# Kernel optimization log

Measured on AMD Instinct MI355X. Metric: run time of the kernel, lower is better.

The kernel has to match this reference:

```python
import jax, jax.numpy as jnp
import numpy as np

N_NODES = 32_000
N_EDGES = 512_000
D_NODE_IN = 3
D_EDGE_IN = 3
LATENT = 32
HIDDEN = 128
MP_ITERS = 4
D_OUT = 1


def _w(key, shape):
    # fan-in scaled init (lecun-normal-ish), fan_in is the second-to-last dim
    return jax.random.normal(key, shape, jnp.float32) / jnp.sqrt(jnp.float32(shape[-2]))


def _mlp(x, w0, w1, w2):
    # MLP with nb_layers=2 hidden relu layers + linear output, no biases
    return jax.nn.relu(jax.nn.relu(x @ w0) @ w1) @ w2


def setup_inputs() -> dict:
    key = jax.random.key(0)
    ks = jax.random.split(key, 32)
    inp = {
        "input_node": jax.random.normal(ks[0], (N_NODES, D_NODE_IN), jnp.float32),
        "input_edge": jax.random.normal(ks[1], (N_EDGES, D_EDGE_IN), jnp.float32),
        "graph_index": jax.random.randint(ks[2], (N_EDGES, 2), 0, N_NODES, jnp.int32),
        # node encoder: D_NODE_IN -> H -> H -> LATENT
        "enc_n_w0": _w(ks[3], (D_NODE_IN, HIDDEN)),
        "enc_n_w1": _w(ks[4], (HIDDEN, HIDDEN)),
        "enc_n_w2": _w(ks[5], (HIDDEN, LATENT)),
        # edge encoder: D_EDGE_IN -> H -> H -> LATENT
        "enc_e_w0": _w(ks[6], (D_EDGE_IN, HIDDEN)),
        "enc_e_w1": _w(ks[7], (HIDDEN, HIDDEN)),
        "enc_e_w2": _w(ks[8], (HIDDEN, LATENT)),
        # per-iteration edge processor MLP: 3*LATENT -> H -> H -> LATENT (stacked over MP_ITERS)
        "ep_w0": _w(ks[9], (MP_ITERS, 3 * LATENT, HIDDEN)),
        "ep_w1": _w(ks[10], (MP_ITERS, HIDDEN, HIDDEN)),
        "ep_w2": _w(ks[11], (MP_ITERS, HIDDEN, LATENT)),
        # per-iteration node processor MLP: 2*LATENT -> H -> H -> LATENT
        "np_w0": _w(ks[12], (MP_ITERS, 2 * LATENT, HIDDEN)),
        "np_w1": _w(ks[13], (MP_ITERS, HIDDEN, HIDDEN)),
        "np_w2": _w(ks[14], (MP_ITERS, HIDDEN, LATENT)),
        # node decoder: LATENT -> H -> H -> D_OUT
        "dec_w0": _w(ks[15], (LATENT, HIDDEN)),
        "dec_w1": _w(ks[16], (HIDDEN, HIDDEN)),
        "dec_w2": _w(ks[17], (HIDDEN, D_OUT)),
    }
    return inp


def reference(input_node, input_edge, graph_index,
              enc_n_w0, enc_n_w1, enc_n_w2,
              enc_e_w0, enc_e_w1, enc_e_w2,
              ep_w0, ep_w1, ep_w2,
              np_w0, np_w1, np_w2,
              dec_w0, dec_w1, dec_w2):
    senders = graph_index[:, 0]
    receivers = graph_index[:, 1]
    n_nodes = input_node.shape[0]

    node = _mlp(input_node, enc_n_w0, enc_n_w1, enc_n_w2)  # [N, LATENT]
    edge = _mlp(input_edge, enc_e_w0, enc_e_w1, enc_e_w2)  # [E, LATENT]

    def step(carry, ws):
        node, edge = carry
        ew0, ew1, ew2, nw0, nw1, nw2 = ws
        # edge update: concat(edge, node[sender], node[receiver]) -> MLP -> residual
        e_in = jnp.concatenate([edge, node[senders], node[receivers]], axis=-1)
        edge = _mlp(e_in, ew0, ew1, ew2) + edge
        # jraph aggregates edges to nodes; NodeProcessor uses only received aggregation
        recv_agg = jax.ops.segment_sum(edge, receivers, num_segments=n_nodes)
        n_in = jnp.concatenate([node, recv_agg], axis=-1)
        node = _mlp(n_in, nw0, nw1, nw2) + node
        return (node, edge), None

    (node, edge), _ = jax.lax.scan(
        step, (node, edge), (ep_w0, ep_w1, ep_w2, np_w0, np_w1, np_w2))

    return _mlp(node, dec_w0, dec_w1, dec_w2)  # [N, D_OUT]
```

## Files before the change

### kernel.cpp

```cpp
#include <hip/hip_runtime.h>

typedef __attribute__((ext_vector_type(8))) _Float16 f16x8;
typedef __attribute__((ext_vector_type(4))) _Float16 f16x4;
typedef __attribute__((ext_vector_type(4))) float f32x4;

#define DI __device__ __forceinline__
#define BAR() asm volatile("s_waitcnt lgkmcnt(0)\n\ts_barrier" ::: "memory")

DI f32x4 mfma16(f16x8 a, f16x8 b, f32x4 c) {
    return __builtin_amdgcn_mfma_f32_16x16x32_f16(a, b, c, 0, 0, 0);
}


template <int NK>
DI void load_wf2(const _Float16* __restrict__ wt, int Kp, int nbase, int l16, int q,
                 f16x8 f[NK][2]) {
#pragma unroll
    for (int nt = 0; nt < 2; ++nt) {
        int n = nbase + nt * 16 + l16;
#pragma unroll
        for (int ks = 0; ks < NK; ++ks)
            f[ks][nt] = *(const f16x8*)(wt + n * Kp + ks * 32 + q * 8);
    }
}

template <int NK0, int MH>
DI void l01(const f16x8 (*w0f)[2], const f16x8 (*w1f)[2],
            const _Float16* __restrict__ X, int xstride,
            _Float16* __restrict__ H0, _Float16* __restrict__ H1,
            int l16, int w, int q) {
    const f32x4 zero = {0.f, 0.f, 0.f, 0.f};
    f32x4 acc[2][MH];
#pragma unroll
    for (int nt = 0; nt < 2; ++nt)
#pragma unroll
        for (int mt = 0; mt < MH; ++mt) acc[nt][mt] = zero;
#pragma unroll
    for (int ks = 0; ks < NK0; ++ks) {
        f16x8 x[MH];
#pragma unroll
        for (int mt = 0; mt < MH; ++mt)
            x[mt] = *(const f16x8*)(X + (mt * 16 + l16) * xstride + ks * 32 + q * 8);
#pragma unroll
        for (int nt = 0; nt < 2; ++nt)
#pragma unroll
            for (int mt = 0; mt < MH; ++mt)
                acc[nt][mt] = mfma16(w0f[ks][nt], x[mt], acc[nt][mt]);
    }
#pragma unroll
    for (int mt = 0; mt < MH; ++mt)
#pragma unroll
        for (int nt = 0; nt < 2; ++nt) {
            f16x4 h;
#pragma unroll
            for (int i = 0; i < 4; ++i) h[i] = (_Float16)fmaxf(acc[nt][mt][i], 0.f);
            *(f16x4*)(H0 + (mt * 16 + l16) * 136 + w * 32 + nt * 16 + q * 4) = h;
        }
    BAR();
    f32x4 a1[2][MH];
#pragma unroll
    for (int nt = 0; nt < 2; ++nt)
#pragma unroll
        for (int mt = 0; mt < MH; ++mt) a1[nt][mt] = zero;
#pragma unroll
    for (int ks = 0; ks < 4; ++ks) {
        f16x8 x[MH];
#pragma unroll
        for (int mt = 0; mt < MH; ++mt)
            x[mt] = *(const f16x8*)(H0 + (mt * 16 + l16) * 136 + ks * 32 + q * 8);
#pragma unroll
        for (int nt = 0; nt < 2; ++nt)
#pragma unroll
            for (int mt = 0; mt < MH; ++mt)
                a1[nt][mt] = mfma16(w1f[ks][nt], x[mt], a1[nt][mt]);
    }
#pragma unroll
    for (int mt = 0; mt < MH; ++mt)
#pragma unroll
        for (int nt = 0; nt < 2; ++nt) {
            f16x4 h;
#pragma unroll
            for (int i = 0; i < 4; ++i) h[i] = (_Float16)fmaxf(a1[nt][mt][i], 0.f);
            *(f16x4*)(H1 + (mt * 16 + l16) * 136 + w * 32 + nt * 16 + q * 4) = h;
        }
    BAR();
}

DI f32x4 l2g(const f16x8* w2f, const _Float16* __restrict__ H1, int l16, int w,
             int q, int g) {
    int m = (w >> 1) * 16 + l16 + 32 * g;
    f32x4 acc = {0.f, 0.f, 0.f, 0.f};
#pragma unroll
    for (int ks = 0; ks < 4; ++ks) {
        f16x8 x = *(const f16x8*)(H1 + m * 136 + ks * 32 + q * 8);
        acc = mfma16(w2f[ks], x, acc);
    }
    return acc;
}

struct WPtrs { const float* p[15]; };

__global__ void k_prep(WPtrs wp, _Float16* __restrict__ ws) {
    int b = blockIdx.x;
    const float* src; int K, N, Np, Kp, off;
    if (b == 0)       { src = wp.p[0];  K = 3;   N = 128; Np = 128; Kp = 32;  off = 0; }
    else if (b == 1)  { src = wp.p[1];  K = 128; N = 128; Np = 128; Kp = 128; off = 4096; }
    else if (b == 2)  { src = wp.p[2];  K = 128; N = 32;  Np = 32;  Kp = 128; off = 20480; }
    else if (b == 3)  { src = wp.p[3];  K = 3;   N = 128; Np = 128; Kp = 32;  off = 24576; }
    else if (b == 4)  { src = wp.p[4];  K = 128; N = 128; Np = 128; Kp = 128; off = 28672; }
    else if (b == 5)  { src = wp.p[5];  K = 128; N = 32;  Np = 32;  Kp = 128; off = 45056; }
    else if (b <= 9)  { int t = b - 6;  src = wp.p[6] + t * 12288;  K = 96;  N = 128; Np = 128; Kp = 96;  off = 49152 + t * 32768; }
    else if (b <= 13) { int t = b - 10; src = wp.p[7] + t * 16384;  K = 128; N = 128; Np = 128; Kp = 128; off = 61440 + t * 32768; }
    else if (b <= 17) { int t = b - 14; src = wp.p[8] + t * 4096;   K = 128; N = 32;  Np = 32;  Kp = 128; off = 77824 + t * 32768; }
    else if (b <= 21) { int t = b - 18; src = wp.p[9] + t * 8192;   K = 64;  N = 128; Np = 128; Kp = 64;  off = 180224 + t * 28672; }
    else if (b <= 25) { int t = b - 22; src = wp.p[10] + t * 16384; K = 128; N = 128; Np = 128; Kp = 128; off = 188416 + t * 28672; }
    else if (b <= 29) { int t = b - 26; src = wp.p[11] + t * 4096;  K = 128; N = 32;  Np = 32;  Kp = 128; off = 204800 + t * 28672; }
    else if (b == 30) { src = wp.p[12]; K = 32;  N = 128; Np = 128; Kp = 32;  off = 294912; }
    else if (b == 31) { src = wp.p[13]; K = 128; N = 128; Np = 128; Kp = 128; off = 299008; }
    else              { src = wp.p[14]; K = 128; N = 1;   Np = 16;  Kp = 128; off = 315392; }
    int total = Np * Kp;
    for (int i = threadIdx.x; i < total; i += 256) {
        int n = i / Kp, k = i - n * Kp;
        float v = (k < K && n < N) ? src[k * N + n] : 0.f;
        ws[off + i] = (_Float16)v;
    }
}

__global__ void k_zero(unsigned* __restrict__ p, int n) {
    int i = blockIdx.x * 256 + threadIdx.x;
    if (i < n) p[i] = 0u;
}
__global__ void k_hist(const int* __restrict__ gi, unsigned* __restrict__ cnt) {
    int e = blockIdx.x * 256 + threadIdx.x;
    if (e < 512000) atomicAdd(&cnt[gi[2 * e + 1]], 1u);
}
__global__ __launch_bounds__(1024) void k_scan(
    const unsigned* __restrict__ cnt, unsigned* __restrict__ rowptr,
    unsigned* __restrict__ cursor) {
    __shared__ unsigned s[1024];
    int t = threadIdx.x;
    unsigned loc[32];
    unsigned sum = 0;
#pragma unroll
    for (int i = 0; i < 32; ++i) {
        int idx = t * 32 + i;
        unsigned v = (idx < 32000) ? cnt[idx] : 0u;
        loc[i] = v; sum += v;
    }
    s[t] = sum;
    __syncthreads();
#pragma unroll
    for (int d = 1; d < 1024; d <<= 1) {
        unsigned x = (t >= d) ? s[t - d] : 0u;
        __syncthreads();
        s[t] += x;
        __syncthreads();
    }
    if (t == 1023) rowptr[32000] = s[1023];
    unsigned off = (t == 0) ? 0u : s[t - 1];
#pragma unroll
    for (int i = 0; i < 32; ++i) {
        int idx = t * 32 + i;
        if (idx < 32000) { rowptr[idx] = off; cursor[idx] = off; off += loc[i]; }
    }
}
__global__ void k_scatter(const int* __restrict__ gi, unsigned* __restrict__ cursor,
                          unsigned* __restrict__ iperm, int2* __restrict__ sr) {
    int e = blockIdx.x * 256 + threadIdx.x;
    if (e < 512000) {
        int s = gi[2 * e], r = gi[2 * e + 1];
        unsigned pos = atomicAdd(&cursor[r], 1u);
        iperm[pos] = (unsigned)e;
        sr[pos] = make_int2(s, r);
    }
}

__global__ __launch_bounds__(256, 3) void k_enc(
    const float* __restrict__ in, _Float16* __restrict__ out,
    const _Float16* __restrict__ w0t, const _Float16* __restrict__ w1t,
    const _Float16* __restrict__ w2t, int NT, const unsigned* __restrict__ iperm) {
    __shared__ __align__(16) _Float16 Xp[64 * 40];
    __shared__ __align__(16) _Float16 H0[64 * 136];
    __shared__ __align__(16) _Float16 H1[64 * 136];
    const int tid = threadIdx.x, w = tid >> 6, lane = tid & 63;
    const int q = lane >> 4, l16 = lane & 15;
    f16x8 w0f[1][2], w1f[4][2], w2f[4];
    load_wf2<1>(w0t, 32, w * 32, l16, q, w0f);
    load_wf2<4>(w1t, 128, w * 32, l16, q, w1f);
    {
        int n2 = (w & 1) * 16 + l16;
#pragma unroll
        for (int ks = 0; ks < 4; ++ks)
            w2f[ks] = *(const f16x8*)(w2t + n2 * 128 + ks * 32 + q * 8);
    }
    for (int c = tid; c < 2560; c += 256) Xp[c] = (_Float16)0.f;
    BAR();

    const int g = gridDim.x;
    const int dr = tid / 3, dc = tid - dr * 3;
    const int orow = (w >> 1) * 16 + l16, ocol = (w & 1) * 16 + q * 4;
    int t = blockIdx.x;

    while (true) {
        if (tid < 192) {
            unsigned e = iperm ? iperm[t * 64 + dr] : (unsigned)(t * 64 + dr);
            Xp[dr * 40 + dc] = (_Float16)in[e * 3 + dc];
        }
        BAR();
        l01<1, 4>(w0f, w1f, Xp, 40, H0, H1, l16, w, q);
#pragma unroll
        for (int gg = 0; gg < 2; ++gg) {
            f32x4 o = l2g(w2f, H1, l16, w, q, gg);
            f16x4 ov;
#pragma unroll
            for (int i = 0; i < 4; ++i) ov[i] = (_Float16)o[i];
            *(f16x4*)(out + (t * 64 + gg * 32 + orow) * 32 + ocol) = ov;
        }
        t += g;
        if (t >= NT) break;
    }
}

__global__ __launch_bounds__(256, 3) void k_edge(
    const _Float16* __restrict__ node, _Float16* __restrict__ edgeP,
    const int2* __restrict__ sr,
    const _Float16* __restrict__ w0t, const _Float16* __restrict__ w1t,
    const _Float16* __restrict__ w2t) {
    __shared__ __align__(16) _Float16 Xe[64 * 104];
    __shared__ __align__(16) _Float16 H0[64 * 136];
    __shared__ __align__(16) _Float16 H1[64 * 136];
    const int tid = threadIdx.x, w = tid >> 6, lane = tid & 63;
    const int q = lane >> 4, l16 = lane & 15;
    f16x8 w0f[3][2], w1f[4][2], w2f[4];
    load_wf2<3>(w0t, 96, w * 32, l16, q, w0f);
    load_wf2<4>(w1t, 128, w * 32, l16, q, w1f);
    {
        int n2 = (w & 1) * 16 + l16;
#pragma unroll
        for (int ks = 0; ks < 4; ++ks)
            w2f[ks] = *(const f16x8*)(w2t + n2 * 128 + ks * 32 + q * 8);
    }
    int cr[3], cs[3];
#pragma unroll
    for (int j = 0; j < 3; ++j) {
        int c = tid + 256 * j;
        cr[j] = c / 12; cs[j] = c - cr[j] * 12;
    }
    const int orow = (w >> 1) * 16 + l16, ocol = (w & 1) * 16 + q * 4;

    const int NT = 8000, g = gridDim.x;
    int t = blockIdx.x;
    int2 srv[3];
#pragma unroll
    for (int j = 0; j < 3; ++j) srv[j] = sr[t * 64 + cr[j]];

    while (true) {
        int tn = t + g; if (tn >= NT) tn = t;
        int4 v[3];
#pragma unroll
        for (int j = 0; j < 3; ++j) {
            int s = cs[j];
            const _Float16* src = (s < 4) ? edgeP + (t * 64 + cr[j]) * 32 + s * 8
                               : (s < 8) ? node + srv[j].x * 32 + (s - 4) * 8
                                         : node + srv[j].y * 32 + (s - 8) * 8;
            v[j] = *(const int4*)src;
        }
        int2 srn[3];
#pragma unroll
        for (int j = 0; j < 3; ++j) srn[j] = sr[tn * 64 + cr[j]];
#pragma unroll
        for (int j = 0; j < 3; ++j)
            *(int4*)(Xe + cr[j] * 104 + cs[j] * 8) = v[j];
        BAR();
        f16x4 oldv[2];
#pragma unroll
        for (int gg = 0; gg < 2; ++gg)
            oldv[gg] = *(const f16x4*)(Xe + (gg * 32 + orow) * 104 + ocol);

        l01<3, 4>(w0f, w1f, Xe, 104, H0, H1, l16, w, q);
#pragma unroll
        for (int gg = 0; gg < 2; ++gg) {
            f32x4 o = l2g(w2f, H1, l16, w, q, gg);
            f16x4 nv;
#pragma unroll
            for (int i = 0; i < 4; ++i) nv[i] = (_Float16)(o[i] + (float)oldv[gg][i]);
            *(f16x4*)(edgeP + (t * 64 + gg * 32 + orow) * 32 + ocol) = nv;
        }

        if (tn == t) break;
        t = tn;
#pragma unroll
        for (int j = 0; j < 3; ++j) srv[j] = srn[j];
    }
}

__global__ __launch_bounds__(256, 3) void k_node(
    _Float16* __restrict__ node, const _Float16* __restrict__ edgeP,
    const unsigned* __restrict__ rowptr,
    const _Float16* __restrict__ w0t, const _Float16* __restrict__ w1t,
    const _Float16* __restrict__ w2t) {
    __shared__ __align__(16) _Float16 Xn[32 * 72];
    __shared__ __align__(16) _Float16 H0[32 * 136];
    __shared__ __align__(16) _Float16 H1[32 * 136];
    const int tid = threadIdx.x, w = tid >> 6, lane = tid & 63;
    const int q = lane >> 4, l16 = lane & 15;
    f16x8 w0f[2][2], w1f[4][2], w2f[4];
    load_wf2<2>(w0t, 64, w * 32, l16, q, w0f);
    load_wf2<4>(w1t, 128, w * 32, l16, q, w1f);
    {
        int n2 = (w & 1) * 16 + l16;
#pragma unroll
        for (int ks = 0; ks < 4; ++ks)
            w2f[ks] = *(const f16x8*)(w2t + n2 * 128 + ks * 32 + q * 8);
    }
    const int t = blockIdx.x;
    const int orow = (w >> 1) * 16 + l16, ocol = (w & 1) * 16 + q * 4;
    {
        int cr = tid >> 3, cs = tid & 7;
        int r = t * 32 + cr;
        if (cs < 4) {
            *(int4*)(Xn + cr * 72 + cs * 8) = *(const int4*)(node + r * 32 + cs * 8);
        } else {
            unsigned b = rowptr[r], e = rowptr[r + 1];
            const _Float16* base = edgeP + (cs - 4) * 8;
            float a0[8], a1[8];
#pragma unroll
            for (int i = 0; i < 8; ++i) { a0[i] = 0.f; a1[i] = 0.f; }
            unsigned p = b;
            for (; p + 2 <= e; p += 2) {
                f16x8 x0 = *(const f16x8*)(base + (p + 0) * 32);
                f16x8 x1 = *(const f16x8*)(base + (p + 1) * 32);
#pragma unroll
                for (int i = 0; i < 8; ++i) { a0[i] += (float)x0[i]; a1[i] += (float)x1[i]; }
            }
            if (p < e) {
                f16x8 x0 = *(const f16x8*)(base + p * 32);
#pragma unroll
                for (int i = 0; i < 8; ++i) a0[i] += (float)x0[i];
            }
            f16x8 h;
#pragma unroll
            for (int i = 0; i < 8; ++i) h[i] = (_Float16)(a0[i] + a1[i]);
            *(f16x8*)(Xn + cr * 72 + cs * 8) = h;
        }
    }
    BAR();
    f16x4 oldv = *(const f16x4*)(Xn + orow * 72 + ocol);
    l01<2, 2>(w0f, w1f, Xn, 72, H0, H1, l16, w, q);
    f32x4 o = l2g(w2f, H1, l16, w, q, 0);
    f16x4 nv;
#pragma unroll
    for (int i = 0; i < 4; ++i) nv[i] = (_Float16)(o[i] + (float)oldv[i]);
    *(f16x4*)(node + (t * 32 + orow) * 32 + ocol) = nv;
}

__global__ __launch_bounds__(256, 3) void k_dec(
    const _Float16* __restrict__ node,
    const _Float16* __restrict__ w0t, const _Float16* __restrict__ w1t,
    const _Float16* __restrict__ w2t, float* __restrict__ out) {
    __shared__ __align__(16) _Float16 Xd[64 * 40];
    __shared__ __align__(16) _Float16 H0[64 * 136];
    __shared__ __align__(16) _Float16 H1[64 * 136];
    const int tid = threadIdx.x, w = tid >> 6, lane = tid & 63;
    const int q = lane >> 4, l16 = lane & 15;
    f16x8 w0f[1][2], w1f[4][2], w2f[4];
    load_wf2<1>(w0t, 32, w * 32, l16, q, w0f);
    load_wf2<4>(w1t, 128, w * 32, l16, q, w1f);
    {
        int n2 = l16;
#pragma unroll
        for (int ks = 0; ks < 4; ++ks)
            w2f[ks] = *(const f16x8*)(w2t + n2 * 128 + ks * 32 + q * 8);
    }
    const int t = blockIdx.x;
    {
        int cr = tid >> 2, cs = tid & 3;
        *(int4*)(Xd + cr * 40 + cs * 8) = *(const int4*)(node + (t * 64 + cr) * 32 + cs * 8);
    }
    BAR();
    l01<1, 4>(w0f, w1f, Xd, 40, H0, H1, l16, w, q);
#pragma unroll
    for (int gg = 0; gg < 2; ++gg) {
        f32x4 o = l2g(w2f, H1, l16, w, q, gg);
        if ((w & 1) == 0 && q == 0) out[t * 64 + gg * 32 + (w >> 1) * 16 + l16] = o[0];
    }
}

extern "C" void kernel_launch(void* const* d_in, const int* in_sizes, int n_in,
                              void* d_out, int out_size, void* d_ws, size_t ws_size,
                              hipStream_t stream) {
    const float* input_node = (const float*)d_in[0];
    const float* input_edge = (const float*)d_in[1];
    const int* gi = (const int*)d_in[2];

    _Float16* ws = (_Float16*)d_ws;
    _Float16* node = (_Float16*)((char*)d_ws + 655360);
    _Float16* edgeP = (_Float16*)((char*)d_ws + 2703360);
    unsigned* rowptr = (unsigned*)((char*)d_ws + 35471360);
    unsigned* cursor = (unsigned*)((char*)d_ws + 35599616);
    unsigned* iperm = (unsigned*)((char*)d_ws + 35727616);
    int2* sr = (int2*)((char*)d_ws + 37775616);

    WPtrs wp;
    for (int i = 0; i < 15; ++i) wp.p[i] = (const float*)d_in[3 + i];

    k_prep<<<33, 256, 0, stream>>>(wp, ws);

    k_zero<<<125, 256, 0, stream>>>(cursor, 32000);
    k_hist<<<2000, 256, 0, stream>>>(gi, cursor);
    k_scan<<<1, 1024, 0, stream>>>(cursor, rowptr, cursor);
    k_scatter<<<2000, 256, 0, stream>>>(gi, cursor, iperm, sr);

    k_enc<<<500, 256, 0, stream>>>(input_node, node, ws + 0, ws + 4096, ws + 20480,
                                   500, nullptr);
    k_enc<<<768, 256, 0, stream>>>(input_edge, edgeP, ws + 24576, ws + 28672,
                                   ws + 45056, 8000, iperm);

    for (int t = 0; t < 4; ++t) {
        k_edge<<<768, 256, 0, stream>>>(node, edgeP, sr,
                                        ws + 49152 + t * 32768,
                                        ws + 61440 + t * 32768,
                                        ws + 77824 + t * 32768);
        k_node<<<1000, 256, 0, stream>>>(node, edgeP, rowptr,
                                         ws + 180224 + t * 28672,
                                         ws + 188416 + t * 28672,
                                         ws + 204800 + t * 28672);
    }
    k_dec<<<500, 256, 0, stream>>>(node, ws + 294912, ws + 299008, ws + 315392,
                                   (float*)d_out);
}
```

Before: 503.9 us.

## Alias input staging buffer onto H1 LDS to raise occupancy to 4 blocks/CU

Each MLP kernel now stages its input tile in the H1 shared buffer instead of a separate LDS array, cutting LDS per block so launch bounds can ask for 4 blocks per CU. Grids grow to 1024 for the edge kernels. The node kernel moves to 64-row tiles so it shares the same LDS layout. Because the staging buffer is reused, the persistent loops need an extra barrier per tile, and k_edge drops its prefetch of the next tile's sender/receiver indices. The extra occupancy is meant to hide the latency of the gathers and global loads, at the cost of more register pressure and lost prefetch.

```diff
diff --git a/kernel.cpp b/kernel.cpp
--- a/kernel.cpp
+++ b/kernel.cpp
@@ -175,13 +175,13 @@
     }
 }
 
-__global__ __launch_bounds__(256, 3) void k_enc(
+__global__ __launch_bounds__(256, 4) void k_enc(
     const float* __restrict__ in, _Float16* __restrict__ out,
     const _Float16* __restrict__ w0t, const _Float16* __restrict__ w1t,
     const _Float16* __restrict__ w2t, int NT, const unsigned* __restrict__ iperm) {
-    __shared__ __align__(16) _Float16 Xp[64 * 40];
     __shared__ __align__(16) _Float16 H0[64 * 136];
-    __shared__ __align__(16) _Float16 H1[64 * 136];
+    __shared__ __align__(16) _Float16 H1s[64 * 136];
+    _Float16* const Xp = H1s;
     const int tid = threadIdx.x, w = tid >> 6, lane = tid & 63;
     const int q = lane >> 4, l16 = lane & 15;
     f16x8 w0f[1][2], w1f[4][2], w2f[4];
@@ -193,24 +193,27 @@
         for (int ks = 0; ks < 4; ++ks)
             w2f[ks] = *(const f16x8*)(w2t + n2 * 128 + ks * 32 + q * 8);
     }
-    for (int c = tid; c < 2560; c += 256) Xp[c] = (_Float16)0.f;
-    BAR();
-
     const int g = gridDim.x;
-    const int dr = tid / 3, dc = tid - dr * 3;
+    const int cr = tid >> 2, csx = tid & 3;
     const int orow = (w >> 1) * 16 + l16, ocol = (w & 1) * 16 + q * 4;
     int t = blockIdx.x;
 
     while (true) {
-        if (tid < 192) {
-            unsigned e = iperm ? iperm[t * 64 + dr] : (unsigned)(t * 64 + dr);
-            Xp[dr * 40 + dc] = (_Float16)in[e * 3 + dc];
-        }
+        f16x8 h;
+#pragma unroll
+        for (int i = 0; i < 8; ++i) h[i] = (_Float16)0.f;
+        if (csx == 0) {
+            unsigned e = iperm ? iperm[t * 64 + cr] : (unsigned)(t * 64 + cr);
+            h[0] = (_Float16)in[e * 3 + 0];
+            h[1] = (_Float16)in[e * 3 + 1];
+            h[2] = (_Float16)in[e * 3 + 2];
+        }
+        *(f16x8*)(Xp + cr * 40 + csx * 8) = h;
         BAR();
-        l01<1, 4>(w0f, w1f, Xp, 40, H0, H1, l16, w, q);
+        l01<1, 4>(w0f, w1f, Xp, 40, H0, H1s, l16, w, q);
 #pragma unroll
         for (int gg = 0; gg < 2; ++gg) {
-            f32x4 o = l2g(w2f, H1, l16, w, q, gg);
+            f32x4 o = l2g(w2f, H1s, l16, w, q, gg);
             f16x4 ov;
 #pragma unroll
             for (int i = 0; i < 4; ++i) ov[i] = (_Float16)o[i];
@@ -218,17 +221,18 @@
         }
         t += g;
         if (t >= NT) break;
-    }
-}
-
-__global__ __launch_bounds__(256, 3) void k_edge(
+        BAR();
+    }
+}
+
+__global__ __launch_bounds__(256, 4) void k_edge(
     const _Float16* __restrict__ node, _Float16* __restrict__ edgeP,
     const int2* __restrict__ sr,
     const _Float16* __restrict__ w0t, const _Float16* __restrict__ w1t,
     const _Float16* __restrict__ w2t) {
-    __shared__ __align__(16) _Float16 Xe[64 * 104];
     __shared__ __align__(16) _Float16 H0[64 * 136];
-    __shared__ __align__(16) _Float16 H1[64 * 136];
+    __shared__ __align__(16) _Float16 H1s[64 * 136];
+    _Float16* const Xe = H1s;
     const int tid = threadIdx.x, w = tid >> 6, lane = tid & 63;
     const int q = lane >> 4, l16 = lane & 15;
     f16x8 w0f[3][2], w1f[4][2], w2f[4];
@@ -250,12 +254,11 @@
 
     const int NT = 8000, g = gridDim.x;
     int t = blockIdx.x;
-    int2 srv[3];
-#pragma unroll
-    for (int j = 0; j < 3; ++j) srv[j] = sr[t * 64 + cr[j]];
 
     while (true) {
-        int tn = t + g; if (tn >= NT) tn = t;
+        int2 srv[3];
+#pragma unroll
+        for (int j = 0; j < 3; ++j) srv[j] = sr[t * 64 + cr[j]];
         int4 v[3];
 #pragma unroll
         for (int j = 0; j < 3; ++j) {
@@ -265,9 +268,6 @@
                                          : node + srv[j].y * 32 + (s - 8) * 8;
             v[j] = *(const int4*)src;
         }
-        int2 srn[3];
-#pragma unroll
-        for (int j = 0; j < 3; ++j) srn[j] = sr[tn * 64 + cr[j]];
 #pragma unroll
         for (int j = 0; j < 3; ++j)
             *(int4*)(Xe + cr[j] * 104 + cs[j] * 8) = v[j];
@@ -277,31 +277,30 @@
         for (int gg = 0; gg < 2; ++gg)
             oldv[gg] = *(const f16x4*)(Xe + (gg * 32 + orow) * 104 + ocol);
 
-        l01<3, 4>(w0f, w1f, Xe, 104, H0, H1, l16, w, q);
+        l01<3, 4>(w0f, w1f, Xe, 104, H0, H1s, l16, w, q);
 #pragma unroll
         for (int gg = 0; gg < 2; ++gg) {
-            f32x4 o = l2g(w2f, H1, l16, w, q, gg);
+            f32x4 o = l2g(w2f, H1s, l16, w, q, gg);
             f16x4 nv;
 #pragma unroll
             for (int i = 0; i < 4; ++i) nv[i] = (_Float16)(o[i] + (float)oldv[gg][i]);
             *(f16x4*)(edgeP + (t * 64 + gg * 32 + orow) * 32 + ocol) = nv;
         }
 
-        if (tn == t) break;
-        t = tn;
-#pragma unroll
-        for (int j = 0; j < 3; ++j) srv[j] = srn[j];
-    }
-}
-
-__global__ __launch_bounds__(256, 3) void k_node(
+        t += g;
+        if (t >= NT) break;
+        BAR();
+    }
+}
+
+__global__ __launch_bounds__(256, 4) void k_node(
     _Float16* __restrict__ node, const _Float16* __restrict__ edgeP,
     const unsigned* __restrict__ rowptr,
     const _Float16* __restrict__ w0t, const _Float16* __restrict__ w1t,
     const _Float16* __restrict__ w2t) {
-    __shared__ __align__(16) _Float16 Xn[32 * 72];
-    __shared__ __align__(16) _Float16 H0[32 * 136];
-    __shared__ __align__(16) _Float16 H1[32 * 136];
+    __shared__ __align__(16) _Float16 H0[64 * 136];
+    __shared__ __align__(16) _Float16 H1s[64 * 136];
+    _Float16* const Xn = H1s;
     const int tid = threadIdx.x, w = tid >> 6, lane = tid & 63;
     const int q = lane >> 4, l16 = lane & 15;
     f16x8 w0f[2][2], w1f[4][2], w2f[4];
@@ -315,9 +314,11 @@
     }
     const int t = blockIdx.x;
     const int orow = (w >> 1) * 16 + l16, ocol = (w & 1) * 16 + q * 4;
-    {
-        int cr = tid >> 3, cs = tid & 7;
-        int r = t * 32 + cr;
+#pragma unroll
+    for (int j = 0; j < 2; ++j) {
+        int c = tid + 256 * j;
+        int cr = c >> 3, cs = c & 7;
+        int r = t * 64 + cr;
         if (cs < 4) {
             *(int4*)(Xn + cr * 72 + cs * 8) = *(const int4*)(node + r * 32 + cs * 8);
         } else {
@@ -345,22 +346,28 @@
         }
     }
     BAR();
-    f16x4 oldv = *(const f16x4*)(Xn + orow * 72 + ocol);
-    l01<2, 2>(w0f, w1f, Xn, 72, H0, H1, l16, w, q);
-    f32x4 o = l2g(w2f, H1, l16, w, q, 0);
-    f16x4 nv;
-#pragma unroll
-    for (int i = 0; i < 4; ++i) nv[i] = (_Float16)(o[i] + (float)oldv[i]);
-    *(f16x4*)(node + (t * 32 + orow) * 32 + ocol) = nv;
-}
-
-__global__ __launch_bounds__(256, 3) void k_dec(
+    f16x4 oldv[2];
+#pragma unroll
+    for (int gg = 0; gg < 2; ++gg)
+        oldv[gg] = *(const f16x4*)(Xn + (gg * 32 + orow) * 72 + ocol);
+    l01<2, 4>(w0f, w1f, Xn, 72, H0, H1s, l16, w, q);
+#pragma unroll
+    for (int gg = 0; gg < 2; ++gg) {
+        f32x4 o = l2g(w2f, H1s, l16, w, q, gg);
+        f16x4 nv;
+#pragma unroll
+        for (int i = 0; i < 4; ++i) nv[i] = (_Float16)(o[i] + (float)oldv[gg][i]);
+        *(f16x4*)(node + (t * 64 + gg * 32 + orow) * 32 + ocol) = nv;
+    }
+}
+
+__global__ __launch_bounds__(256, 4) void k_dec(
     const _Float16* __restrict__ node,
     const _Float16* __restrict__ w0t, const _Float16* __restrict__ w1t,
     const _Float16* __restrict__ w2t, float* __restrict__ out) {
-    __shared__ __align__(16) _Float16 Xd[64 * 40];
     __shared__ __align__(16) _Float16 H0[64 * 136];
-    __shared__ __align__(16) _Float16 H1[64 * 136];
+    __shared__ __align__(16) _Float16 H1s[64 * 136];
+    _Float16* const Xd = H1s;
     const int tid = threadIdx.x, w = tid >> 6, lane = tid & 63;
     const int q = lane >> 4, l16 = lane & 15;
     f16x8 w0f[1][2], w1f[4][2], w2f[4];
@@ -378,10 +385,10 @@
         *(int4*)(Xd + cr * 40 + cs * 8) = *(const int4*)(node + (t * 64 + cr) * 32 + cs * 8);
     }
     BAR();
-    l01<1, 4>(w0f, w1f, Xd, 40, H0, H1, l16, w, q);
+    l01<1, 4>(w0f, w1f, Xd, 40, H0, H1s, l16, w, q);
 #pragma unroll
     for (int gg = 0; gg < 2; ++gg) {
-        f32x4 o = l2g(w2f, H1, l16, w, q, gg);
+        f32x4 o = l2g(w2f, H1s, l16, w, q, gg);
         if ((w & 1) == 0 && q == 0) out[t * 64 + gg * 32 + (w >> 1) * 16 + l16] = o[0];
     }
 }
@@ -413,18 +420,18 @@
 
     k_enc<<<500, 256, 0, stream>>>(input_node, node, ws + 0, ws + 4096, ws + 20480,
                                    500, nullptr);
-    k_enc<<<768, 256, 0, stream>>>(input_edge, edgeP, ws + 24576, ws + 28672,
-                                   ws + 45056, 8000, iperm);
+    k_enc<<<1024, 256, 0, stream>>>(input_edge, edgeP, ws + 24576, ws + 28672,
+                                    ws + 45056, 8000, iperm);
 
     for (int t = 0; t < 4; ++t) {
-        k_edge<<<768, 256, 0, stream>>>(node, edgeP, sr,
-                                        ws + 49152 + t * 32768,
-                                        ws + 61440 + t * 32768,
-                                        ws + 77824 + t * 32768);
-        k_node<<<1000, 256, 0, stream>>>(node, edgeP, rowptr,
-                                         ws + 180224 + t * 28672,
-                                         ws + 188416 + t * 28672,
-                                         ws + 204800 + t * 28672);
+        k_edge<<<1024, 256, 0, stream>>>(node, edgeP, sr,
+                                         ws + 49152 + t * 32768,
+                                         ws + 61440 + t * 32768,
+                                         ws + 77824 + t * 32768);
+        k_node<<<500, 256, 0, stream>>>(node, edgeP, rowptr,
+                                        ws + 180224 + t * 28672,
+                                        ws + 188416 + t * 28672,
+                                        ws + 204800 + t * 28672);
     }
     k_dec<<<500, 256, 0, stream>>>(node, ws + 294912, ws + 299008, ws + 315392,
                                    (float*)d_out);
```

Measured after the change: 609.6 us. 21.0% more time.

## Prefetch next edge tile into LDS with async global_load_lds during layer 1

Applied to the files above, without the earlier changes.

The edge kernel now gathers the edge, sender-node and receiver-node features with direct global-to-LDS loads (global_load_lds) rather than loading into registers and storing to shared memory. The gather for the next tile is issued right after layer 0 of the current tile, so it overlaps the layer-1 and layer-2 matrix work. A vmcnt wait was added to the barrier at the top of the loop. Staging is remapped to 13 16-byte chunks per row to match the 104-element row stride, with the pad chunk filled by a dummy load. The shared MLP layer helper is split into separate layer-0 and layer-1 functions so the prefetch can sit between them.

```diff
diff --git a/kernel.cpp b/kernel.cpp
--- a/kernel.cpp
+++ b/kernel.cpp
@@ -6,9 +6,16 @@
 
 #define DI __device__ __forceinline__
 #define BAR() asm volatile("s_waitcnt lgkmcnt(0)\n\ts_barrier" ::: "memory")
+#define BARV() asm volatile("s_waitcnt vmcnt(0) lgkmcnt(0)\n\ts_barrier" ::: "memory")
 
 DI f32x4 mfma16(f16x8 a, f16x8 b, f32x4 c) {
     return __builtin_amdgcn_mfma_f32_16x16x32_f16(a, b, c, 0, 0, 0);
+}
+
+DI void glds16(const void* g, void* l) {
+    __builtin_amdgcn_global_load_lds(
+        (const __attribute__((address_space(1))) void*)g,
+        (__attribute__((address_space(3))) void*)l, 16, 0, 0);
 }
 
 
@@ -22,6 +29,70 @@
         for (int ks = 0; ks < NK; ++ks)
             f[ks][nt] = *(const f16x8*)(wt + n * Kp + ks * 32 + q * 8);
     }
+}
+
+template <int NK0, int MH>
+DI void l0_run(const f16x8 (*w0f)[2], const _Float16* __restrict__ X, int xstride,
+               _Float16* __restrict__ H0, int l16, int w, int q) {
+    const f32x4 zero = {0.f, 0.f, 0.f, 0.f};
+    f32x4 acc[2][MH];
+#pragma unroll
+    for (int nt = 0; nt < 2; ++nt)
+#pragma unroll
+        for (int mt = 0; mt < MH; ++mt) acc[nt][mt] = zero;
+#pragma unroll
+    for (int ks = 0; ks < NK0; ++ks) {
+        f16x8 x[MH];
+#pragma unroll
+        for (int mt = 0; mt < MH; ++mt)
+            x[mt] = *(const f16x8*)(X + (mt * 16 + l16) * xstride + ks * 32 + q * 8);
+#pragma unroll
+        for (int nt = 0; nt < 2; ++nt)
+#pragma unroll
+            for (int mt = 0; mt < MH; ++mt)
+                acc[nt][mt] = mfma16(w0f[ks][nt], x[mt], acc[nt][mt]);
+    }
+#pragma unroll
+    for (int mt = 0; mt < MH; ++mt)
+#pragma unroll
+        for (int nt = 0; nt < 2; ++nt) {
+            f16x4 h;
+#pragma unroll
+            for (int i = 0; i < 4; ++i) h[i] = (_Float16)fmaxf(acc[nt][mt][i], 0.f);
+            *(f16x4*)(H0 + (mt * 16 + l16) * 136 + w * 32 + nt * 16 + q * 4) = h;
+        }
+}
+
+template <int MH>
+DI void l1_run(const f16x8 (*w1f)[2], const _Float16* __restrict__ H0,
+               _Float16* __restrict__ H1, int l16, int w, int q) {
+    const f32x4 zero = {0.f, 0.f, 0.f, 0.f};
+    f32x4 a1[2][MH];
+#pragma unroll
+    for (int nt = 0; nt < 2; ++nt)
+#pragma unroll
+        for (int mt = 0; mt < MH; ++mt) a1[nt][mt] = zero;
+#pragma unroll
+    for (int ks = 0; ks < 4; ++ks) {
+        f16x8 x[MH];
+#pragma unroll
+        for (int mt = 0; mt < MH; ++mt)
+            x[mt] = *(const f16x8*)(H0 + (mt * 16 + l16) * 136 + ks * 32 + q * 8);
+#pragma unroll
+        for (int nt = 0; nt < 2; ++nt)
+#pragma unroll
+            for (int mt = 0; mt < MH; ++mt)
+                a1[nt][mt] = mfma16(w1f[ks][nt], x[mt], a1[nt][mt]);
+    }
+#pragma unroll
+    for (int mt = 0; mt < MH; ++mt)
+#pragma unroll
+        for (int nt = 0; nt < 2; ++nt) {
+            f16x4 h;
+#pragma unroll
+            for (int i = 0; i < 4; ++i) h[i] = (_Float16)fmaxf(a1[nt][mt][i], 0.f);
+            *(f16x4*)(H1 + (mt * 16 + l16) * 136 + w * 32 + nt * 16 + q * 4) = h;
+        }
 }
 
 template <int NK0, int MH>
@@ -29,60 +100,9 @@
             const _Float16* __restrict__ X, int xstride,
             _Float16* __restrict__ H0, _Float16* __restrict__ H1,
             int l16, int w, int q) {
-    const f32x4 zero = {0.f, 0.f, 0.f, 0.f};
-    f32x4 acc[2][MH];
-#pragma unroll
-    for (int nt = 0; nt < 2; ++nt)
-#pragma unroll
-        for (int mt = 0; mt < MH; ++mt) acc[nt][mt] = zero;
-#pragma unroll
-    for (int ks = 0; ks < NK0; ++ks) {
-        f16x8 x[MH];
-#pragma unroll
-        for (int mt = 0; mt < MH; ++mt)
-            x[mt] = *(const f16x8*)(X + (mt * 16 + l16) * xstride + ks * 32 + q * 8);
-#pragma unroll
-        for (int nt = 0; nt < 2; ++nt)
-#pragma unroll
-            for (int mt = 0; mt < MH; ++mt)
-                acc[nt][mt] = mfma16(w0f[ks][nt], x[mt], acc[nt][mt]);
-    }
-#pragma unroll
-    for (int mt = 0; mt < MH; ++mt)
-#pragma unroll
-        for (int nt = 0; nt < 2; ++nt) {
-            f16x4 h;
-#pragma unroll
-            for (int i = 0; i < 4; ++i) h[i] = (_Float16)fmaxf(acc[nt][mt][i], 0.f);
-            *(f16x4*)(H0 + (mt * 16 + l16) * 136 + w * 32 + nt * 16 + q * 4) = h;
-        }
+    l0_run<NK0, MH>(w0f, X, xstride, H0, l16, w, q);
     BAR();
-    f32x4 a1[2][MH];
-#pragma unroll
-    for (int nt = 0; nt < 2; ++nt)
-#pragma unroll
-        for (int mt = 0; mt < MH; ++mt) a1[nt][mt] = zero;
-#pragma unroll
-    for (int ks = 0; ks < 4; ++ks) {
-        f16x8 x[MH];
-#pragma unroll
-        for (int mt = 0; mt < MH; ++mt)
-            x[mt] = *(const f16x8*)(H0 + (mt * 16 + l16) * 136 + ks * 32 + q * 8);
-#pragma unroll
-        for (int nt = 0; nt < 2; ++nt)
-#pragma unroll
-            for (int mt = 0; mt < MH; ++mt)
-                a1[nt][mt] = mfma16(w1f[ks][nt], x[mt], a1[nt][mt]);
-    }
-#pragma unroll
-    for (int mt = 0; mt < MH; ++mt)
-#pragma unroll
-        for (int nt = 0; nt < 2; ++nt) {
-            f16x4 h;
-#pragma unroll
-            for (int i = 0; i < 4; ++i) h[i] = (_Float16)fmaxf(a1[nt][mt][i], 0.f);
-            *(f16x4*)(H1 + (mt * 16 + l16) * 136 + w * 32 + nt * 16 + q * 4) = h;
-        }
+    l1_run<MH>(w1f, H0, H1, l16, w, q);
     BAR();
 }
 
@@ -240,44 +260,46 @@
         for (int ks = 0; ks < 4; ++ks)
             w2f[ks] = *(const f16x8*)(w2t + n2 * 128 + ks * 32 + q * 8);
     }
-    int cr[3], cs[3];
-#pragma unroll
-    for (int j = 0; j < 3; ++j) {
-        int c = tid + 256 * j;
-        cr[j] = c / 12; cs[j] = c - cr[j] * 12;
+    int sm[4], sc[4];
+#pragma unroll
+    for (int i = 0; i < 4; ++i) {
+        int s = 256 * i + tid;
+        int m = (s * 5042) >> 16;
+        sm[i] = m; sc[i] = s - m * 13;
     }
     const int orow = (w >> 1) * 16 + l16, ocol = (w & 1) * 16 + q * 4;
-
     const int NT = 8000, g = gridDim.x;
+
+    auto stage = [&](int tt) {
+#pragma unroll
+        for (int i = 0; i < 4; ++i) {
+            if (i < 3 || tid < 64) {
+                int m = sm[i], cc = sc[i];
+                int2 p = sr[tt * 64 + m];
+                const _Float16* src;
+                if (cc < 4)       src = edgeP + (tt * 64 + m) * 32 + cc * 8;
+                else if (cc < 8)  src = node + p.x * 32 + (cc - 4) * 8;
+                else if (cc < 12) src = node + p.y * 32 + (cc - 8) * 8;
+                else              src = edgeP + (tt * 64 + m) * 32;
+                glds16(src, Xe + (i * 256 + w * 64) * 8);
+            }
+        }
+    };
+
     int t = blockIdx.x;
-    int2 srv[3];
-#pragma unroll
-    for (int j = 0; j < 3; ++j) srv[j] = sr[t * 64 + cr[j]];
-
+    stage(t);
     while (true) {
         int tn = t + g; if (tn >= NT) tn = t;
-        int4 v[3];
-#pragma unroll
-        for (int j = 0; j < 3; ++j) {
-            int s = cs[j];
-            const _Float16* src = (s < 4) ? edgeP + (t * 64 + cr[j]) * 32 + s * 8
-                               : (s < 8) ? node + srv[j].x * 32 + (s - 4) * 8
-                                         : node + srv[j].y * 32 + (s - 8) * 8;
-            v[j] = *(const int4*)src;
-        }
-        int2 srn[3];
-#pragma unroll
-        for (int j = 0; j < 3; ++j) srn[j] = sr[tn * 64 + cr[j]];
-#pragma unroll
-        for (int j = 0; j < 3; ++j)
-            *(int4*)(Xe + cr[j] * 104 + cs[j] * 8) = v[j];
-        BAR();
+        BARV();
         f16x4 oldv[2];
 #pragma unroll
         for (int gg = 0; gg < 2; ++gg)
             oldv[gg] = *(const f16x4*)(Xe + (gg * 32 + orow) * 104 + ocol);
-
-        l01<3, 4>(w0f, w1f, Xe, 104, H0, H1, l16, w, q);
+        l0_run<3, 4>(w0f, Xe, 104, H0, l16, w, q);
+        BAR();
+        if (tn != t) stage(tn);
+        l1_run<4>(w1f, H0, H1, l16, w, q);
+        BAR();
 #pragma unroll
         for (int gg = 0; gg < 2; ++gg) {
             f32x4 o = l2g(w2f, H1, l16, w, q, gg);
@@ -286,11 +308,8 @@
             for (int i = 0; i < 4; ++i) nv[i] = (_Float16)(o[i] + (float)oldv[gg][i]);
             *(f16x4*)(edgeP + (t * 64 + gg * 32 + orow) * 32 + ocol) = nv;
         }
-
         if (tn == t) break;
         t = tn;
-#pragma unroll
-        for (int j = 0; j < 3; ++j) srv[j] = srn[j];
     }
 }
 
```

Measured after the change: 526.4 us. +4.5%, slower.
